# Kernel tuning notes

Hardware: AMD Instinct MI355X
Metric: run time of the kernel (lower is better)

Reference implementation:

```python
import jax, jax.numpy as jnp
import numpy as np

B = 16        # graphs per batch
N0 = 4096     # nodes per graph (equal-size graphs -> static TopK shapes)
DEG = 8       # avg degree
E = B * N0 * DEG
CW = 64
OUT = 256


def _seg_sum(vals, idx, n):
    return jax.ops.segment_sum(vals, idx, num_segments=n)


def _sage(x, src, dst, valid, wl, bl, wr, n):
    # PyG SAGEConv: lin_l(mean_{j->i} x_j) + lin_r(x_i); lin_r has no bias
    vf = valid.astype(x.dtype)
    msg = x[src] * vf[:, None]                     # [E, d]
    s = _seg_sum(msg, dst, n)
    cnt = _seg_sum(vf, dst, n)
    mean = s / jnp.maximum(cnt, 1.0)[:, None]
    return mean @ wl.T + bl + x @ wr.T


def _gcn(x, src, dst, valid, w, b, n):
    # PyG GCNConv: add self-loops, symmetric normalization
    h = x @ w.T
    vf = valid.astype(x.dtype)
    deg = 1.0 + _seg_sum(vf, dst, n)               # includes self-loop
    inv_sqrt = jax.lax.rsqrt(deg)
    norm = inv_sqrt[src] * inv_sqrt[dst] * vf      # [E]
    agg = _seg_sum(h[src] * norm[:, None], dst, n) + h * (1.0 / deg)[:, None]
    return agg + b


def _topk_pool(x, src, dst, valid, w, n_per_graph):
    # PyG TopKPooling: score = x@w/||w||, keep top ceil(ratio*n) per graph,
    # x' = x[perm] * tanh(score[perm]); reindex edges, drop edges with removed endpoints.
    k = (n_per_graph + 1) // 2
    score = (x @ w) / jnp.linalg.norm(w)
    vals, idx = jax.lax.top_k(score.reshape(B, n_per_graph), k)   # [B,k]
    offs = (jnp.arange(B, dtype=jnp.int32) * n_per_graph)[:, None]
    perm = (idx.astype(jnp.int32) + offs).reshape(-1)             # [B*k] global ids
    x_new = x[perm] * jnp.tanh(vals.reshape(-1))[:, None]
    new_idx = jnp.full((B * n_per_graph,), -1, dtype=jnp.int32).at[perm].set(
        jnp.arange(B * k, dtype=jnp.int32))
    s2, d2 = new_idx[src], new_idx[dst]
    valid2 = valid & (s2 >= 0) & (d2 >= 0)
    s2 = jnp.where(valid2, s2, 0)
    d2 = jnp.where(valid2, d2, 0)
    return x_new, s2, d2, valid2, k


def _readout(x, k):
    xg = x.reshape(B, k, -1)
    return jnp.concatenate([xg.max(axis=1), xg.mean(axis=1)], axis=1)  # [B, 2d]


def _forward(x, edge_src, edge_dst, w1_l, b1, w1_r, w2_l, b2, w2_r, w3_l, b3, w3_r,
             w4, b4, w5, b5, w6, b6, p1, p2, p3, p4, p5, p6,
             lw1, lb1, lw2, lb2, lw3, lb3):
    src, dst = edge_src, edge_dst
    valid = jnp.ones((E,), dtype=bool)
    n = N0
    sage_ps = [(w1_l, b1, w1_r), (w2_l, b2, w2_r), (w3_l, b3, w3_r)]
    gcn_ps = [(w4, b4), (w5, b5), (w6, b6)]
    pools = [p1, p2, p3, p4, p5, p6]
    h = x
    z = None
    for i in range(6):
        if i < 3:
            wl, bl, wr = sage_ps[i]
            h = jax.nn.relu(_sage(h, src, dst, valid, wl, bl, wr, B * n))
        else:
            w, b = gcn_ps[i - 3]
            h = jax.nn.relu(_gcn(h, src, dst, valid, w, b, B * n))
        h, src, dst, valid, n = _topk_pool(h, src, dst, valid, pools[i], n)
        r = _readout(h, n)
        z = r if z is None else z + r
    z = jax.nn.relu(z @ lw1.T + lb1)
    z = jax.nn.relu(z @ lw2.T + lb2)
    z = z @ lw3.T + lb3
    return jax.nn.softmax(z, axis=1)


def setup_inputs() -> dict:
    key = jax.random.key(0)
    ks = jax.random.split(key, 40)

    def nrm(k, shape, s=0.1):
        return jax.random.normal(k, shape, dtype=jnp.float32) * s

    # per-graph random edges (both endpoints inside the same graph block)
    epg = N0 * DEG
    src_l = jax.random.randint(ks[0], (B, epg), 0, N0, dtype=jnp.int32)
    dst_l = jax.random.randint(ks[1], (B, epg), 0, N0, dtype=jnp.int32)
    offs = (jnp.arange(B, dtype=jnp.int32) * N0)[:, None]
    inp = {
        'x': jax.random.normal(ks[2], (B * N0, 2), dtype=jnp.float32),
        'edge_src': (src_l + offs).reshape(-1),
        'edge_dst': (dst_l + offs).reshape(-1),
        'w1_l': nrm(ks[3], (CW, 2)), 'b1': nrm(ks[4], (CW,)), 'w1_r': nrm(ks[5], (CW, 2)),
        'w2_l': nrm(ks[6], (CW, CW)), 'b2': nrm(ks[7], (CW,)), 'w2_r': nrm(ks[8], (CW, CW)),
        'w3_l': nrm(ks[9], (CW, CW)), 'b3': nrm(ks[10], (CW,)), 'w3_r': nrm(ks[11], (CW, CW)),
        'w4': nrm(ks[12], (CW, CW)), 'b4': jnp.zeros((CW,), jnp.float32),
        'w5': nrm(ks[13], (CW, CW)), 'b5': jnp.zeros((CW,), jnp.float32),
        'w6': nrm(ks[14], (CW, CW)), 'b6': jnp.zeros((CW,), jnp.float32),
        'p1': nrm(ks[15], (CW,)), 'p2': nrm(ks[16], (CW,)), 'p3': nrm(ks[17], (CW,)),
        'p4': nrm(ks[18], (CW,)), 'p5': nrm(ks[19], (CW,)), 'p6': nrm(ks[20], (CW,)),
        'lw1': nrm(ks[21], (128, 2 * CW)), 'lb1': nrm(ks[22], (128,)),
        'lw2': nrm(ks[23], (64, 128)), 'lb2': nrm(ks[24], (64,)),
        'lw3': nrm(ks[25], (OUT, 64)), 'lb3': nrm(ks[26], (OUT,)),
    }
    return inp


def reference(x, edge_src, edge_dst, w1_l, b1, w1_r, w2_l, b2, w2_r, w3_l, b3, w3_r,
              w4, b4, w5, b5, w6, b6, p1, p2, p3, p4, p5, p6,
              lw1, lb1, lw2, lb2, lw3, lb3):
    return _forward(x, edge_src, edge_dst, w1_l, b1, w1_r, w2_l, b2, w2_r,
                    w3_l, b3, w3_r, w4, b4, w5, b5, w6, b6,
                    p1, p2, p3, p4, p5, p6, lw1, lb1, lw2, lb2, lw3, lb3)
```

## Files before the change

kernel.cpp:

```cpp
#include <hip/hip_runtime.h>
#include <math.h>

#define NB 16
#define N0 4096
#define NE 524288
#define CAPE 1280


static __global__ void k_count(const int* __restrict__ dst, int* __restrict__ cnt) {
  int e = blockIdx.x * 256 + threadIdx.x;
  if (e >= NE) return;
  atomicAdd(&cnt[dst[e]], 1);
}

static __global__ void k_fill0(const int* __restrict__ src, const int* __restrict__ dst,
                               int* __restrict__ cursor, int* __restrict__ list) {
  int e = blockIdx.x * 256 + threadIdx.x;
  if (e >= NE) return;
  int d = dst[e];
  int slot = atomicAdd(&cursor[d], 1);
  list[slot] = src[e];
}


static __global__ void k_scan1(const int* __restrict__ in, int* __restrict__ out,
                               int* __restrict__ bsum, int n) {
  __shared__ int ts[256];
  int base = blockIdx.x * 1024 + threadIdx.x * 4;
  int a0 = (base + 0 < n) ? in[base + 0] : 0;
  int a1 = (base + 1 < n) ? in[base + 1] : 0;
  int a2 = (base + 2 < n) ? in[base + 2] : 0;
  int a3 = (base + 3 < n) ? in[base + 3] : 0;
  int s = a0 + a1 + a2 + a3;
  ts[threadIdx.x] = s;
  __syncthreads();
  for (int off = 1; off < 256; off <<= 1) {
    int v = (threadIdx.x >= off) ? ts[threadIdx.x - off] : 0;
    __syncthreads();
    ts[threadIdx.x] += v;
    __syncthreads();
  }
  int excl = ts[threadIdx.x] - s;
  if (base + 0 < n) out[base + 0] = excl;
  excl += a0;
  if (base + 1 < n) out[base + 1] = excl;
  excl += a1;
  if (base + 2 < n) out[base + 2] = excl;
  excl += a2;
  if (base + 3 < n) out[base + 3] = excl;
  if (threadIdx.x == 255) bsum[blockIdx.x] = ts[255];
}

static __global__ void k_scan2(int* __restrict__ bsum, int nb) {
  __shared__ int t[64];
  int i = threadIdx.x;
  int v = (i < nb) ? bsum[i] : 0;
  t[i] = v;
  __syncthreads();
  for (int off = 1; off < 64; off <<= 1) {
    int u = (i >= off) ? t[i - off] : 0;
    __syncthreads();
    t[i] += u;
    __syncthreads();
  }
  if (i < nb) bsum[i] = t[i] - v;
}

static __global__ void k_scan3(int* __restrict__ out, int* __restrict__ out2,
                               const int* __restrict__ bsum, int n) {
  int i = blockIdx.x * 256 + threadIdx.x;
  if (i < n) {
    int v = out[i] + bsum[i >> 10];
    out[i] = v;
    if (out2) out2[i] = v;
  }
}


static __global__ void k_newcount(const int* __restrict__ perm, const int* __restrict__ offs,
                                  const int* __restrict__ cnt, const int* __restrict__ list,
                                  const int* __restrict__ newidx, int* __restrict__ ncnt,
                                  int newn) {
  int nn = blockIdx.x * 256 + threadIdx.x;
  if (nn >= newn) return;
  int old = perm[nn];
  int st = offs[old], c = cnt[old];
  int cc = 0;
  for (int j = 0; j < c; ++j) cc += (newidx[list[st + j]] >= 0);
  ncnt[nn] = cc;
}

static __global__ void k_newfill(const int* __restrict__ perm, const int* __restrict__ offs,
                                 const int* __restrict__ cnt, const int* __restrict__ list,
                                 const int* __restrict__ newidx, const int* __restrict__ noffs,
                                 int* __restrict__ nlist, int newn) {
  int nn = blockIdx.x * 256 + threadIdx.x;
  if (nn >= newn) return;
  int old = perm[nn];
  int st = offs[old], c = cnt[old];
  int pos = noffs[nn];
  for (int j = 0; j < c; ++j) {
    int s2 = newidx[list[st + j]];
    if (s2 >= 0) nlist[pos++] = s2;
  }
}


static __global__ void k_pnorm(const float* __restrict__ p0, const float* __restrict__ p1,
                               const float* __restrict__ p2, const float* __restrict__ p3,
                               const float* __restrict__ p4, const float* __restrict__ p5,
                               float* __restrict__ pnbuf) {
  const float* pp = p0;
  switch (blockIdx.x) {
    case 1: pp = p1; break;
    case 2: pp = p2; break;
    case 3: pp = p3; break;
    case 4: pp = p4; break;
    case 5: pp = p5; break;
    default: break;
  }
  double v = (double)pp[threadIdx.x];
  v *= v;
#pragma unroll
  for (int off = 1; off < 64; off <<= 1) v += __shfl_xor(v, off);
  if (threadIdx.x == 0) pnbuf[blockIdx.x] = (float)(1.0 / sqrt(v));
}


static __global__ void k_wprep(const float* __restrict__ w0, const float* __restrict__ w1,
                               const float* __restrict__ w2, const float* __restrict__ w3,
                               const float* __restrict__ w4, const float* __restrict__ w5,
                               const float* __restrict__ w6, float* __restrict__ wp) {
  const float* src = w0;
  switch (blockIdx.x) {
    case 1: src = w1; break;
    case 2: src = w2; break;
    case 3: src = w3; break;
    case 4: src = w4; break;
    case 5: src = w5; break;
    case 6: src = w6; break;
    default: break;
  }
  float* dst = wp + (size_t)blockIdx.x * 4096;
  const float4* w4p = (const float4*)src;
  for (int i4 = threadIdx.x; i4 < 1024; i4 += 256) {
    int o = i4 >> 4, db = (i4 & 15) << 2;
    float4 W = w4p[i4];
    float Wv[4] = {W.x, W.y, W.z, W.w};
    int og = o >> 2, o3 = o & 3;
#pragma unroll
    for (int j = 0; j < 4; ++j) {
      int d = db + j;
      dst[(d << 6) + (((og ^ (d & 15)) << 2) | o3)] = Wv[j];
    }
  }
}


static __global__ void k_sage_gather2(const float* __restrict__ x, const int* __restrict__ offs,
                                      const int* __restrict__ cnt, const int* __restrict__ list,
                                      float* __restrict__ mean, int ntot) {
  int v = blockIdx.x * 256 + threadIdx.x;
  if (v >= ntot) return;
  int st = offs[v], c = cnt[v];
  float s0 = 0.f, s1 = 0.f;
  for (int j = 0; j < c; ++j) {
    int s = list[st + j];
    s0 += x[s * 2 + 0];
    s1 += x[s * 2 + 1];
  }
  float inv = 1.0f / fmaxf((float)c, 1.0f);
  mean[v * 2 + 0] = s0 * inv;
  mean[v * 2 + 1] = s1 * inv;
}

static __global__ void k_sage0(const float* __restrict__ x, const float* __restrict__ mean,
                               const float* __restrict__ wl, const float* __restrict__ blv,
                               const float* __restrict__ wr, const float* __restrict__ pvec,
                               const float* __restrict__ pnbuf, float* __restrict__ h,
                               float* __restrict__ score, int ntot) {
  __shared__ float wlT[2][65], wrT[2][65];
  if (threadIdx.x < 128) {
    int o = threadIdx.x >> 1, d = threadIdx.x & 1;
    wlT[d][o] = wl[o * 2 + d];
    wrT[d][o] = wr[o * 2 + d];
  }
  __syncthreads();
  int o = threadIdx.x & 63, vl = threadIdx.x >> 6;
  int base = blockIdx.x * 16 + vl * 4;
  float pn = pnbuf[0];
  float psl = pvec[o];
#pragma unroll
  for (int r = 0; r < 4; ++r) {
    int v = base + r;
    if (v >= ntot) break;
    float acc = blv[o] + mean[v * 2 + 0] * wlT[0][o] + mean[v * 2 + 1] * wlT[1][o] +
                x[v * 2 + 0] * wrT[0][o] + x[v * 2 + 1] * wrT[1][o];
    float hval = fmaxf(acc, 0.0f);
    h[(size_t)v * 64 + o] = hval;
    double sc = (double)hval * (double)psl;
#pragma unroll
    for (int off = 1; off < 64; off <<= 1) sc += __shfl_xor(sc, off);
    if (o == 0) score[v] = (float)sc * pn;
  }
}

static __global__ __launch_bounds__(256) void k_sage_mm(
    const float* __restrict__ x, const int* __restrict__ offs, const int* __restrict__ cnt,
    const int* __restrict__ list, const float* __restrict__ wlT, const float* __restrict__ blv,
    const float* __restrict__ wrT, const float* __restrict__ pvec,
    const float* __restrict__ pnbuf, int pidx, float* __restrict__ h,
    float* __restrict__ score) {
  __shared__ float smem[8192];
  __shared__ float psh[64], bsh[64];
  __shared__ int lds_list[CAPE];
  float* xT = smem;
  float* mT = smem + 4096;
  int t = threadIdx.x;
  size_t nb = (size_t)((blockIdx.x & 7) * (gridDim.x >> 3) + (blockIdx.x >> 3));

  if (t < 64) {
    psh[t] = pvec[t];
    bsh[t] = blv[t];
  }
  const float4* x4 = (const float4*)(x + nb * 4096);
  for (int i = t; i < 1024; i += 256) {
    int node = i >> 4, db = (i & 15) << 2;
    float4 a = x4[i];
    float av[4] = {a.x, a.y, a.z, a.w};
    int ng = node >> 2, n0 = node & 3;
#pragma unroll
    for (int j = 0; j < 4; ++j) {
      int d = db + j;
      xT[(d << 6) + (((ng ^ (d & 15)) << 2) | n0)] = av[j];
    }
  }
  int gv0 = (int)nb * 64;
  int st0 = offs[gv0];
  int nedge = offs[gv0 + 63] + cnt[gv0 + 63] - st0;
  int ncap = (nedge < CAPE) ? nedge : CAPE;
  for (int e = t; e < ncap; e += 256) lds_list[e] = list[st0 + e];
  __syncthreads();

  {
    int lane = t & 63, w = t >> 6;
    int stq[16], cq[16];
    float accq[16];
    int cmax = 0;
#pragma unroll
    for (int q = 0; q < 16; ++q) {
      int gv = gv0 + w * 16 + q;
      stq[q] = offs[gv] - st0;
      cq[q] = cnt[gv];
      accq[q] = 0.f;
      cmax = max(cmax, cq[q]);
    }
    int ncl = (nedge > 0) ? (nedge - 1) : 0;
    for (int j = 0; j < cmax; ++j) {
#pragma unroll
      for (int q = 0; q < 16; ++q) {
        bool act = j < cq[q];
        int idx = stq[q] + (act ? j : 0);
        idx = (idx < ncl) ? idx : ncl;
        int sn = (idx < ncap) ? lds_list[idx] : list[st0 + idx];
        float xv = x[(size_t)(sn & 32767) * 64 + lane];
        accq[q] = act ? (accq[q] + xv) : accq[q];
      }
    }
#pragma unroll
    for (int q = 0; q < 16; ++q) {
      int node = w * 16 + q;
      float mval = accq[q] * (1.0f / fmaxf((float)cq[q], 1.0f));
      int col = (((node >> 2) ^ (lane & 15)) << 2) | (node & 3);
      mT[(lane << 6) + col] = mval;
    }
  }
  __syncthreads();

  int tx = t & 15, ty = t >> 4;
  float acc[4][4] = {};
#pragma unroll 4
  for (int k = 0; k < 64; ++k) {
    int s = k & 15;
    int ca = (tx ^ s) << 2, cb = (ty ^ s) << 2;
    const float4 a = *(const float4*)&xT[(k << 6) + ca];
    const float4 m = *(const float4*)&mT[(k << 6) + ca];
    const float4 L = *(const float4*)&wlT[(k << 6) + cb];
    const float4 R = *(const float4*)&wrT[(k << 6) + cb];
    float A[4] = {a.x, a.y, a.z, a.w}, M[4] = {m.x, m.y, m.z, m.w};
    float Lv[4] = {L.x, L.y, L.z, L.w}, Rv[4] = {R.x, R.y, R.z, R.w};
#pragma unroll
    for (int r = 0; r < 4; ++r)
#pragma unroll
      for (int c = 0; c < 4; ++c) acc[r][c] += M[r] * Lv[c] + A[r] * Rv[c];
  }

  float pn = pnbuf[pidx];
  float hv[4][4];
  double sp[4];
#pragma unroll
  for (int r = 0; r < 4; ++r) {
    sp[r] = 0.0;
#pragma unroll
    for (int c = 0; c < 4; ++c) {
      float v = fmaxf(acc[r][c] + bsh[(ty << 2) + c], 0.0f);
      hv[r][c] = v;
      sp[r] += (double)v * (double)psh[(ty << 2) + c];
    }
  }
  __syncthreads();
  float* hT = smem;
  double* sred = (double*)(smem + 4608);
#pragma unroll
  for (int r = 0; r < 4; ++r) {
    int node = (tx << 2) + r;
    int nk = node & 15;
#pragma unroll
    for (int c = 0; c < 4; ++c) hT[node * 68 + (((ty ^ nk) << 2) | c)] = hv[r][c];
    sred[(ty << 6) + node] = sp[r];
  }
  __syncthreads();
  float4* h4 = (float4*)(h + nb * 4096);
  for (int i = t; i < 1024; i += 256) {
    int node = i >> 4, q = i & 15;
    h4[i] = *(const float4*)&hT[node * 68 + ((q ^ (node & 15)) << 2)];
  }
  if (t < 64) {
    double ssum = 0.0;
    for (int g = 0; g < 16; ++g) ssum += sred[(g << 6) + t];
    score[nb * 64 + t] = (float)ssum * pn;
  }
}


static __global__ __launch_bounds__(256) void k_gcn_mm(const float* __restrict__ x,
                                                       const float* __restrict__ wT,
                                                       float* __restrict__ h1) {
  __shared__ float smem[4608];
  float* xT = smem;
  int t = threadIdx.x;
  size_t nb = blockIdx.x;
  const float4* x4 = (const float4*)(x + nb * 4096);
  for (int i = t; i < 1024; i += 256) {
    int node = i >> 4, db = (i & 15) << 2;
    float4 a = x4[i];
    float av[4] = {a.x, a.y, a.z, a.w};
    int ng = node >> 2, n0 = node & 3;
#pragma unroll
    for (int j = 0; j < 4; ++j) {
      int d = db + j;
      xT[(d << 6) + (((ng ^ (d & 15)) << 2) | n0)] = av[j];
    }
  }
  __syncthreads();
  int tx = t & 15, ty = t >> 4;
  float acc[4][4] = {};
#pragma unroll 4
  for (int k = 0; k < 64; ++k) {
    int s = k & 15;
    const float4 a = *(const float4*)&xT[(k << 6) + ((tx ^ s) << 2)];
    const float4 W = *(const float4*)&wT[(k << 6) + ((ty ^ s) << 2)];
    float A[4] = {a.x, a.y, a.z, a.w}, Wv[4] = {W.x, W.y, W.z, W.w};
#pragma unroll
    for (int r = 0; r < 4; ++r)
#pragma unroll
      for (int c = 0; c < 4; ++c) acc[r][c] += A[r] * Wv[c];
  }
  __syncthreads();
  float* hT = smem;
#pragma unroll
  for (int r = 0; r < 4; ++r) {
    int node = (tx << 2) + r;
    int nk = node & 15;
#pragma unroll
    for (int c = 0; c < 4; ++c) hT[node * 68 + (((ty ^ nk) << 2) | c)] = acc[r][c];
  }
  __syncthreads();
  float4* h4 = (float4*)(h1 + nb * 4096);
  for (int i = t; i < 1024; i += 256) {
    int node = i >> 4, q = i & 15;
    h4[i] = *(const float4*)&hT[node * 68 + ((q ^ (node & 15)) << 2)];
  }
}

static __global__ void k_gcn_gather(const float* __restrict__ h1, const int* __restrict__ offs,
                                    const int* __restrict__ cnt, const int* __restrict__ list,
                                    const float* __restrict__ b, const float* __restrict__ pvec,
                                    const float* __restrict__ pnbuf, int pidx,
                                    float* __restrict__ h, float* __restrict__ score, int ntot) {
  int lane = threadIdx.x & 63, vl = threadIdx.x >> 6;
  int v = blockIdx.x * 4 + vl;
  if (v >= ntot) return;
  int st = offs[v], c = cnt[v];
  float degv = 1.0f + (float)c;
  float ivd = 1.0f / sqrtf(degv);
  float acc = 0.f;
  for (int j = 0; j < c; ++j) {
    int s = list[st + j];
    float nrm = (1.0f / sqrtf(1.0f + (float)cnt[s])) * ivd;
    acc += h1[(size_t)s * 64 + lane] * nrm;
  }
  float outv = fmaxf(acc + h1[(size_t)v * 64 + lane] * (1.0f / degv) + b[lane], 0.0f);
  h[(size_t)v * 64 + lane] = outv;
  double sc = (double)outv * (double)pvec[lane];
#pragma unroll
  for (int off = 1; off < 64; off <<= 1) sc += __shfl_xor(sc, off);
  if (lane == 0) score[v] = (float)sc * pnbuf[pidx];
}


static __global__ void k_chunksort(const float* __restrict__ score,
                                   unsigned long long* __restrict__ runs, int n_per, int k,
                                   int* __restrict__ newidx, int* __restrict__ perm, int single) {
  extern __shared__ unsigned long long sk[];
  int CH = blockDim.x;
  int g0 = blockIdx.x * CH;
  int b = g0 / n_per;
  int i = threadIdx.x;
  int gi = g0 + i;
  int li = gi - b * n_per;
  unsigned u = __float_as_uint(score[gi]);
  unsigned s = (u & 0x80000000u) ? u : ~(u | 0x80000000u);
  sk[i] = ((unsigned long long)s << 32) | (unsigned)li;
  __syncthreads();
  for (int ksz = 2; ksz <= CH; ksz <<= 1) {
    for (int j = ksz >> 1; j > 0; j >>= 1) {
      int ixj = i ^ j;
      if (ixj > i) {
        unsigned long long a = sk[i], c = sk[ixj];
        bool up = ((i & ksz) == 0);
        if ((a > c) == up) {
          sk[i] = c;
          sk[ixj] = a;
        }
      }
      __syncthreads();
    }
  }
  if (!single) {
    runs[gi] = sk[i];
  } else {
    int r = i;
    int idx = (int)(sk[r] & 0xFFFFFFFFu);
    int gidx = b * n_per + idx;
    if (r < k) {
      perm[b * k + r] = gidx;
      newidx[gidx] = b * k + r;
    } else {
      newidx[gidx] = -1;
    }
  }
}

static __global__ void k_merge(const unsigned long long* __restrict__ in,
                               unsigned long long* __restrict__ out, int L, int ntot, int n_per,
                               int k, int* __restrict__ newidx, int* __restrict__ perm,
                               int final) {
  int g = blockIdx.x * 256 + threadIdx.x;
  if (g >= ntot) return;
  unsigned long long key = in[g];
  int pair = g / (2 * L);
  int base = pair * 2 * L;
  int t = g - base;
  const unsigned long long* sib;
  int p;
  if (t < L) {
    sib = in + base + L;
    p = t;
  } else {
    sib = in + base;
    p = t - L;
  }
  int lo = 0, hi = L;
  while (lo < hi) {
    int mid = (lo + hi) >> 1;
    lo = (sib[mid] < key) ? mid + 1 : lo;
    hi = (sib[mid] < key) ? hi : mid;
  }
  int pos = p + lo;
  if (!final) {
    out[base + pos] = key;
  } else {
    int b = base / n_per;
    int idx = (int)(key & 0xFFFFFFFFu);
    int gidx = b * n_per + idx;
    if (pos < k) {
      perm[b * k + pos] = gidx;
      newidx[gidx] = b * k + pos;
    } else {
      newidx[gidx] = -1;
    }
  }
}


static __global__ __launch_bounds__(1024) void k_gather_ro(
    const float* __restrict__ h, const float* __restrict__ score, const int* __restrict__ perm,
    float* __restrict__ xnew, float* __restrict__ pmax, float* __restrict__ psum) {
  __shared__ float tile[64 * 68];
  __shared__ float pm[16][65], ps[16][65];
  int t = threadIdx.x;
  int node = t >> 4, q = t & 15;
  int nn = blockIdx.x * 64 + node;
  int old = perm[nn];
  float tm = tanhf(score[old]);
  float4 v = *(const float4*)&h[(size_t)old * 64 + q * 4];
  v.x *= tm;
  v.y *= tm;
  v.z *= tm;
  v.w *= tm;
  *(float4*)&xnew[(size_t)nn * 64 + q * 4] = v;
  *(float4*)&tile[node * 68 + ((q ^ (node & 15)) << 2)] = v;
  __syncthreads();
  int slot = t >> 6, d = t & 63;
  int q2 = d >> 2, i3 = d & 3;
  float m = -INFINITY, s = 0.f;
#pragma unroll
  for (int r = 0; r < 4; ++r) {
    int nd = slot * 4 + r;
    float val = tile[nd * 68 + (((q2 ^ (nd & 15)) << 2) | i3)];
    m = fmaxf(m, val);
    s += val;
  }
  pm[slot][d] = m;
  ps[slot][d] = s;
  __syncthreads();
  if (t < 64) {
    float mm = -INFINITY, ss = 0.f;
#pragma unroll
    for (int sl = 0; sl < 16; ++sl) {
      mm = fmaxf(mm, pm[sl][t]);
      ss += ps[sl][t];
    }
    pmax[(size_t)blockIdx.x * 64 + t] = mm;
    psum[(size_t)blockIdx.x * 64 + t] = ss;
  }
}

static __global__ void k_readout_comb(const float* __restrict__ pmax,
                                      const float* __restrict__ psum, float* __restrict__ z,
                                      int k, int nch) {
  int b = blockIdx.x, d = threadIdx.x;
  float m = -INFINITY, s = 0.0f;
  for (int c = 0; c < nch; ++c) {
    m = fmaxf(m, pmax[((size_t)b * nch + c) * 64 + d]);
    s += psum[((size_t)b * nch + c) * 64 + d];
  }
  z[b * 128 + d] += m;
  z[b * 128 + 64 + d] += s / (float)k;
}


static __global__ void k_mlp(const float* __restrict__ z, const float* __restrict__ lw1,
                             const float* __restrict__ lb1, const float* __restrict__ lw2,
                             const float* __restrict__ lb2, const float* __restrict__ lw3,
                             const float* __restrict__ lb3, float* __restrict__ out) {
  __shared__ float zs[128], t1[128], t2[64], t3[256], red[256];
  int b = blockIdx.x, tid = threadIdx.x;
  if (tid < 128) zs[tid] = z[b * 128 + tid];
  __syncthreads();
  if (tid < 128) {
    double a = 0.0;
    for (int d = 0; d < 128; ++d) a += (double)lw1[tid * 128 + d] * (double)zs[d];
    t1[tid] = fmaxf((float)a + lb1[tid], 0.0f);
  }
  __syncthreads();
  if (tid < 64) {
    double a = 0.0;
    for (int d = 0; d < 128; ++d) a += (double)lw2[tid * 128 + d] * (double)t1[d];
    t2[tid] = fmaxf((float)a + lb2[tid], 0.0f);
  }
  __syncthreads();
  {
    double a = 0.0;
    for (int d = 0; d < 64; ++d) a += (double)lw3[tid * 64 + d] * (double)t2[d];
    t3[tid] = (float)a + lb3[tid];
  }
  __syncthreads();
  red[tid] = t3[tid];
  __syncthreads();
  for (int s = 128; s > 0; s >>= 1) {
    if (tid < s) red[tid] = fmaxf(red[tid], red[tid + s]);
    __syncthreads();
  }
  float mx = red[0];
  __syncthreads();
  float e = expf(t3[tid] - mx);
  red[tid] = e;
  __syncthreads();
  for (int s = 128; s > 0; s >>= 1) {
    if (tid < s) red[tid] += red[tid + s];
    __syncthreads();
  }
  out[b * 256 + tid] = e / red[0];
}


extern "C" void kernel_launch(void* const* d_in, const int* in_sizes, int n_in,
                              void* d_out, int out_size, void* d_ws, size_t ws_size,
                              hipStream_t stream) {
  const float* x0 = (const float*)d_in[0];
  const int* esrc0 = (const int*)d_in[1];
  const int* edst0 = (const int*)d_in[2];
  const float* WL[3] = {(const float*)d_in[3], (const float*)d_in[6], (const float*)d_in[9]};
  const float* BL[3] = {(const float*)d_in[4], (const float*)d_in[7], (const float*)d_in[10]};
  const float* WR[3] = {(const float*)d_in[5], (const float*)d_in[8], (const float*)d_in[11]};
  const float* WG[3] = {(const float*)d_in[12], (const float*)d_in[14], (const float*)d_in[16]};
  const float* BG[3] = {(const float*)d_in[13], (const float*)d_in[15], (const float*)d_in[17]};
  const float* P[6] = {(const float*)d_in[18], (const float*)d_in[19], (const float*)d_in[20],
                       (const float*)d_in[21], (const float*)d_in[22], (const float*)d_in[23]};
  const float* lw1 = (const float*)d_in[24];
  const float* lb1 = (const float*)d_in[25];
  const float* lw2 = (const float*)d_in[26];
  const float* lb2 = (const float*)d_in[27];
  const float* lw3 = (const float*)d_in[28];
  const float* lb3 = (const float*)d_in[29];

  char* ws = (char*)d_ws;
  size_t off = 0;
  auto alloc = [&](size_t bytes) -> void* {
    void* p = ws + off;
    off += (bytes + 255) & ~(size_t)255;
    return p;
  };
  float* hA = (float*)alloc((size_t)65536 * 64 * 4);
  float* hB = (float*)alloc((size_t)32768 * 64 * 4);
  float* mean = (float*)alloc((size_t)65536 * 2 * 4);
  float* tmp = (float*)alloc((size_t)8192 * 64 * 4);
  float* score = (float*)alloc((size_t)65536 * 4);
  int* newidx = (int*)alloc((size_t)65536 * 4);
  int* perm = (int*)alloc((size_t)32768 * 4);
  int* cntA = (int*)alloc((size_t)65536 * 4);
  int* cntB = (int*)alloc((size_t)65536 * 4);
  int* offsA = (int*)alloc((size_t)65536 * 4);
  int* offsB = (int*)alloc((size_t)65536 * 4);
  int* cursor = (int*)alloc((size_t)65536 * 4);
  int* bsum = (int*)alloc((size_t)64 * 4);
  int* listA = (int*)alloc((size_t)NE * 4);
  int* listB = (int*)alloc((size_t)NE * 4);
  float* z = (float*)alloc((size_t)16 * 128 * 4);
  float* pmax = (float*)alloc((size_t)NB * 32 * 64 * 4);
  float* psum = (float*)alloc((size_t)NB * 32 * 64 * 4);
  unsigned long long* keyA = (unsigned long long*)alloc((size_t)65536 * 8);
  unsigned long long* keyB = (unsigned long long*)alloc((size_t)65536 * 8);
  float* pnbuf = (float*)alloc((size_t)64 * 4);
  float* wp = (float*)alloc((size_t)7 * 4096 * 4);
  if (off > ws_size) return;

  auto scan = [&](int* cntp, int* offsp, int* curp, int n) {
    int nblk = (n + 1023) / 1024;
    k_scan1<<<nblk, 256, 0, stream>>>(cntp, offsp, bsum, n);
    k_scan2<<<1, 64, 0, stream>>>(bsum, nblk);
    k_scan3<<<(n + 255) / 256, 256, 0, stream>>>(offsp, curp, bsum, n);
  };

  hipMemsetAsync(z, 0, 16 * 128 * 4, stream);
  k_pnorm<<<6, 64, 0, stream>>>(P[0], P[1], P[2], P[3], P[4], P[5], pnbuf);
  k_wprep<<<7, 256, 0, stream>>>(WL[1], WR[1], WL[2], WR[2], WG[0], WG[1], WG[2], wp);

  hipMemsetAsync(cntA, 0, (size_t)65536 * 4, stream);
  k_count<<<NE / 256, 256, 0, stream>>>(edst0, cntA);
  scan(cntA, offsA, cursor, 65536);
  k_fill0<<<NE / 256, 256, 0, stream>>>(esrc0, edst0, cursor, listA);

  const float* xcur = x0;
  int* ccnt = cntA;
  int* coffs = offsA;
  int* clist = listA;

  for (int i = 0; i < 6; ++i) {
    int n_per = N0 >> i;
    int ntot = NB * n_per;
    int k = n_per >> 1;

    if (i == 0) {
      k_sage_gather2<<<(ntot + 255) / 256, 256, 0, stream>>>(xcur, coffs, ccnt, clist, mean, ntot);
      k_sage0<<<(ntot + 15) / 16, 256, 0, stream>>>(xcur, mean, WL[0], BL[0], WR[0], P[0], pnbuf,
                                                    hA, score, ntot);
    } else if (i < 3) {
      const float* wlp = wp + (size_t)((i - 1) * 2 + 0) * 4096;
      const float* wrp = wp + (size_t)((i - 1) * 2 + 1) * 4096;
      k_sage_mm<<<ntot / 64, 256, 0, stream>>>(xcur, coffs, ccnt, clist, wlp, BL[i], wrp, P[i],
                                               pnbuf, i, hA, score);
    } else {
      int g = i - 3;
      k_gcn_mm<<<ntot / 64, 256, 0, stream>>>(xcur, wp + (size_t)(4 + g) * 4096, tmp);
      k_gcn_gather<<<(ntot + 3) / 4, 256, 0, stream>>>(tmp, coffs, ccnt, clist, BG[g], P[i],
                                                       pnbuf, i, hA, score, ntot);
    }

    int CH = (n_per < 1024) ? n_per : 1024;
    int single = (CH == n_per) ? 1 : 0;
    k_chunksort<<<ntot / CH, CH, (size_t)CH * 8, stream>>>(score, keyA, n_per, k, newidx, perm,
                                                           single);
    if (!single) {
      unsigned long long* cur = keyA;
      unsigned long long* nxt = keyB;
      for (int L = CH; L * 2 <= n_per; L <<= 1) {
        int fin = (L * 2 == n_per) ? 1 : 0;
        k_merge<<<(ntot + 255) / 256, 256, 0, stream>>>(cur, nxt, L, ntot, n_per, k, newidx, perm,
                                                        fin);
        unsigned long long* t2 = cur;
        cur = nxt;
        nxt = t2;
      }
    }

    int nch = k / 64;
    k_gather_ro<<<NB * nch, 1024, 0, stream>>>(hA, score, perm, hB, pmax, psum);

    if (i < 5) {
      int newn = NB * k;
      int* ncnt = (i & 1) ? cntA : cntB;
      int* noffs = (i & 1) ? offsA : offsB;
      int* nlist = (i & 1) ? listA : listB;
      k_newcount<<<(newn + 255) / 256, 256, 0, stream>>>(perm, coffs, ccnt, clist, newidx, ncnt,
                                                         newn);
      scan(ncnt, noffs, nullptr, newn);
      k_newfill<<<(newn + 255) / 256, 256, 0, stream>>>(perm, coffs, ccnt, clist, newidx, noffs,
                                                        nlist, newn);
      ccnt = ncnt;
      coffs = noffs;
      clist = nlist;
    }

    k_readout_comb<<<NB, 64, 0, stream>>>(pmax, psum, z, k, nch);
    xcur = hB;
  }

  k_mlp<<<NB, 256, 0, stream>>>(z, lw1, lb1, lw2, lb2, lw3, lb3, (float*)d_out);
}
```

Before: 401.4 us.

## Merge small kernels to cut launches and widen sage_mm blocks to 512 threads

Folds scan2 into scan3 using a wavefront shuffle scan, merges pnorm and wprep into one launch, and merges the newcount work into the pooling gather kernel as extra blocks. Per-level readout combining moves into the final MLP kernel, which also removes the z memset. k_sage_mm now runs 512 threads per block, each thread covering a 2x4 output tile and 8 nodes' gathers instead of 4x4 and 16. The goal is fewer kernel launches and more parallelism in the sage layers, at the cost of some redundant block-sum scans and lower per-thread reuse.

```diff
diff --git a/kernel.cpp b/kernel.cpp
--- a/kernel.cpp
+++ b/kernel.cpp
@@ -51,44 +51,28 @@
   if (threadIdx.x == 255) bsum[blockIdx.x] = ts[255];
 }
 
-static __global__ void k_scan2(int* __restrict__ bsum, int nb) {
-  __shared__ int t[64];
-  int i = threadIdx.x;
-  int v = (i < nb) ? bsum[i] : 0;
-  t[i] = v;
-  __syncthreads();
-  for (int off = 1; off < 64; off <<= 1) {
-    int u = (i >= off) ? t[i - off] : 0;
-    __syncthreads();
-    t[i] += u;
-    __syncthreads();
-  }
-  if (i < nb) bsum[i] = t[i] - v;
-}
-
 static __global__ void k_scan3(int* __restrict__ out, int* __restrict__ out2,
-                               const int* __restrict__ bsum, int n) {
-  int i = blockIdx.x * 256 + threadIdx.x;
+                               const int* __restrict__ bsum, int n, int nblk) {
+  __shared__ int sb[64];
+  int t = threadIdx.x;
+  if (t < 64) {
+    int v = (t < nblk) ? bsum[t] : 0;
+    int p = v;
+    for (int off = 1; off < 64; off <<= 1) {
+      int u = __shfl_up(p, off);
+      if (t >= off) p += u;
+    }
+    sb[t] = p - v;
+  }
+  __syncthreads();
+  int i = blockIdx.x * 256 + t;
   if (i < n) {
-    int v = out[i] + bsum[i >> 10];
+    int v = out[i] + sb[i >> 10];
     out[i] = v;
     if (out2) out2[i] = v;
   }
 }
 
-
-static __global__ void k_newcount(const int* __restrict__ perm, const int* __restrict__ offs,
-                                  const int* __restrict__ cnt, const int* __restrict__ list,
-                                  const int* __restrict__ newidx, int* __restrict__ ncnt,
-                                  int newn) {
-  int nn = blockIdx.x * 256 + threadIdx.x;
-  if (nn >= newn) return;
-  int old = perm[nn];
-  int st = offs[old], c = cnt[old];
-  int cc = 0;
-  for (int j = 0; j < c; ++j) cc += (newidx[list[st + j]] >= 0);
-  ncnt[nn] = cc;
-}
 
 static __global__ void k_newfill(const int* __restrict__ perm, const int* __restrict__ offs,
                                  const int* __restrict__ cnt, const int* __restrict__ list,
@@ -106,52 +90,54 @@
 }
 
 
-static __global__ void k_pnorm(const float* __restrict__ p0, const float* __restrict__ p1,
-                               const float* __restrict__ p2, const float* __restrict__ p3,
-                               const float* __restrict__ p4, const float* __restrict__ p5,
-                               float* __restrict__ pnbuf) {
-  const float* pp = p0;
-  switch (blockIdx.x) {
-    case 1: pp = p1; break;
-    case 2: pp = p2; break;
-    case 3: pp = p3; break;
-    case 4: pp = p4; break;
-    case 5: pp = p5; break;
-    default: break;
-  }
-  double v = (double)pp[threadIdx.x];
-  v *= v;
-#pragma unroll
-  for (int off = 1; off < 64; off <<= 1) v += __shfl_xor(v, off);
-  if (threadIdx.x == 0) pnbuf[blockIdx.x] = (float)(1.0 / sqrt(v));
-}
-
-
-static __global__ void k_wprep(const float* __restrict__ w0, const float* __restrict__ w1,
-                               const float* __restrict__ w2, const float* __restrict__ w3,
-                               const float* __restrict__ w4, const float* __restrict__ w5,
-                               const float* __restrict__ w6, float* __restrict__ wp) {
-  const float* src = w0;
-  switch (blockIdx.x) {
-    case 1: src = w1; break;
-    case 2: src = w2; break;
-    case 3: src = w3; break;
-    case 4: src = w4; break;
-    case 5: src = w5; break;
-    case 6: src = w6; break;
-    default: break;
-  }
-  float* dst = wp + (size_t)blockIdx.x * 4096;
-  const float4* w4p = (const float4*)src;
-  for (int i4 = threadIdx.x; i4 < 1024; i4 += 256) {
-    int o = i4 >> 4, db = (i4 & 15) << 2;
-    float4 W = w4p[i4];
-    float Wv[4] = {W.x, W.y, W.z, W.w};
-    int og = o >> 2, o3 = o & 3;
-#pragma unroll
-    for (int j = 0; j < 4; ++j) {
-      int d = db + j;
-      dst[(d << 6) + (((og ^ (d & 15)) << 2) | o3)] = Wv[j];
+static __global__ void k_pw(const float* __restrict__ p0, const float* __restrict__ p1,
+                            const float* __restrict__ p2, const float* __restrict__ p3,
+                            const float* __restrict__ p4, const float* __restrict__ p5,
+                            const float* __restrict__ w0, const float* __restrict__ w1,
+                            const float* __restrict__ w2, const float* __restrict__ w3,
+                            const float* __restrict__ w4, const float* __restrict__ w5,
+                            const float* __restrict__ w6, float* __restrict__ pnbuf,
+                            float* __restrict__ wp) {
+  if (blockIdx.x < 6) {
+    if (threadIdx.x >= 64) return;
+    const float* pp = p0;
+    switch (blockIdx.x) {
+      case 1: pp = p1; break;
+      case 2: pp = p2; break;
+      case 3: pp = p3; break;
+      case 4: pp = p4; break;
+      case 5: pp = p5; break;
+      default: break;
+    }
+    double v = (double)pp[threadIdx.x];
+    v *= v;
+#pragma unroll
+    for (int off = 1; off < 64; off <<= 1) v += __shfl_xor(v, off);
+    if (threadIdx.x == 0) pnbuf[blockIdx.x] = (float)(1.0 / sqrt(v));
+  } else {
+    int wi = blockIdx.x - 6;
+    const float* src = w0;
+    switch (wi) {
+      case 1: src = w1; break;
+      case 2: src = w2; break;
+      case 3: src = w3; break;
+      case 4: src = w4; break;
+      case 5: src = w5; break;
+      case 6: src = w6; break;
+      default: break;
+    }
+    float* dst = wp + (size_t)wi * 4096;
+    const float4* w4p = (const float4*)src;
+    for (int i4 = threadIdx.x; i4 < 1024; i4 += 256) {
+      int o = i4 >> 4, db = (i4 & 15) << 2;
+      float4 W = w4p[i4];
+      float Wv[4] = {W.x, W.y, W.z, W.w};
+      int og = o >> 2, o3 = o & 3;
+#pragma unroll
+      for (int j = 0; j < 4; ++j) {
+        int d = db + j;
+        dst[(d << 6) + (((og ^ (d & 15)) << 2) | o3)] = Wv[j];
+      }
     }
   }
 }
@@ -205,7 +191,7 @@
   }
 }
 
-static __global__ __launch_bounds__(256) void k_sage_mm(
+static __global__ __launch_bounds__(512) void k_sage_mm(
     const float* __restrict__ x, const int* __restrict__ offs, const int* __restrict__ cnt,
     const int* __restrict__ list, const float* __restrict__ wlT, const float* __restrict__ blv,
     const float* __restrict__ wrT, const float* __restrict__ pvec,
@@ -224,7 +210,7 @@
     bsh[t] = blv[t];
   }
   const float4* x4 = (const float4*)(x + nb * 4096);
-  for (int i = t; i < 1024; i += 256) {
+  for (int i = t; i < 1024; i += 512) {
     int node = i >> 4, db = (i & 15) << 2;
     float4 a = x4[i];
     float av[4] = {a.x, a.y, a.z, a.w};
@@ -239,17 +225,17 @@
   int st0 = offs[gv0];
   int nedge = offs[gv0 + 63] + cnt[gv0 + 63] - st0;
   int ncap = (nedge < CAPE) ? nedge : CAPE;
-  for (int e = t; e < ncap; e += 256) lds_list[e] = list[st0 + e];
+  for (int e = t; e < ncap; e += 512) lds_list[e] = list[st0 + e];
   __syncthreads();
 
   {
     int lane = t & 63, w = t >> 6;
-    int stq[16], cq[16];
-    float accq[16];
+    int stq[8], cq[8];
+    float accq[8];
     int cmax = 0;
 #pragma unroll
-    for (int q = 0; q < 16; ++q) {
-      int gv = gv0 + w * 16 + q;
+    for (int q = 0; q < 8; ++q) {
+      int gv = gv0 + w * 8 + q;
       stq[q] = offs[gv] - st0;
       cq[q] = cnt[gv];
       accq[q] = 0.f;
@@ -258,7 +244,7 @@
     int ncl = (nedge > 0) ? (nedge - 1) : 0;
     for (int j = 0; j < cmax; ++j) {
 #pragma unroll
-      for (int q = 0; q < 16; ++q) {
+      for (int q = 0; q < 8; ++q) {
         bool act = j < cq[q];
         int idx = stq[q] + (act ? j : 0);
         idx = (idx < ncl) ? idx : ncl;
@@ -268,8 +254,8 @@
       }
     }
 #pragma unroll
-    for (int q = 0; q < 16; ++q) {
-      int node = w * 16 + q;
+    for (int q = 0; q < 8; ++q) {
+      int node = w * 8 + q;
       float mval = accq[q] * (1.0f / fmaxf((float)cq[q], 1.0f));
       int col = (((node >> 2) ^ (lane & 15)) << 2) | (node & 3);
       mT[(lane << 6) + col] = mval;
@@ -278,50 +264,51 @@
   __syncthreads();
 
   int tx = t & 15, ty = t >> 4;
-  float acc[4][4] = {};
+  int ng = ty >> 1, n0 = (ty & 1) << 1;
+  float acc[2][4] = {};
 #pragma unroll 4
   for (int k = 0; k < 64; ++k) {
     int s = k & 15;
-    int ca = (tx ^ s) << 2, cb = (ty ^ s) << 2;
-    const float4 a = *(const float4*)&xT[(k << 6) + ca];
-    const float4 m = *(const float4*)&mT[(k << 6) + ca];
-    const float4 L = *(const float4*)&wlT[(k << 6) + cb];
-    const float4 R = *(const float4*)&wrT[(k << 6) + cb];
-    float A[4] = {a.x, a.y, a.z, a.w}, M[4] = {m.x, m.y, m.z, m.w};
+    int ca = (((ng ^ s) << 2) | n0);
+    const float2 a2 = *(const float2*)&xT[(k << 6) + ca];
+    const float2 m2 = *(const float2*)&mT[(k << 6) + ca];
+    const float4 L = *(const float4*)&wlT[(k << 6) + ((tx ^ s) << 2)];
+    const float4 R = *(const float4*)&wrT[(k << 6) + ((tx ^ s) << 2)];
+    float A[2] = {a2.x, a2.y}, M[2] = {m2.x, m2.y};
     float Lv[4] = {L.x, L.y, L.z, L.w}, Rv[4] = {R.x, R.y, R.z, R.w};
 #pragma unroll
-    for (int r = 0; r < 4; ++r)
+    for (int r = 0; r < 2; ++r)
 #pragma unroll
       for (int c = 0; c < 4; ++c) acc[r][c] += M[r] * Lv[c] + A[r] * Rv[c];
   }
 
   float pn = pnbuf[pidx];
-  float hv[4][4];
-  double sp[4];
-#pragma unroll
-  for (int r = 0; r < 4; ++r) {
+  float hv[2][4];
+  double sp[2];
+#pragma unroll
+  for (int r = 0; r < 2; ++r) {
     sp[r] = 0.0;
 #pragma unroll
     for (int c = 0; c < 4; ++c) {
-      float v = fmaxf(acc[r][c] + bsh[(ty << 2) + c], 0.0f);
+      float v = fmaxf(acc[r][c] + bsh[(tx << 2) + c], 0.0f);
       hv[r][c] = v;
-      sp[r] += (double)v * (double)psh[(ty << 2) + c];
+      sp[r] += (double)v * (double)psh[(tx << 2) + c];
     }
   }
   __syncthreads();
   float* hT = smem;
   double* sred = (double*)(smem + 4608);
 #pragma unroll
-  for (int r = 0; r < 4; ++r) {
-    int node = (tx << 2) + r;
+  for (int r = 0; r < 2; ++r) {
+    int node = (ty << 1) + r;
     int nk = node & 15;
 #pragma unroll
-    for (int c = 0; c < 4; ++c) hT[node * 68 + (((ty ^ nk) << 2) | c)] = hv[r][c];
-    sred[(ty << 6) + node] = sp[r];
+    for (int c = 0; c < 4; ++c) hT[node * 68 + (((tx ^ nk) << 2) | c)] = hv[r][c];
+    sred[(tx << 6) + node] = sp[r];
   }
   __syncthreads();
   float4* h4 = (float4*)(h + nb * 4096);
-  for (int i = t; i < 1024; i += 256) {
+  for (int i = t; i < 1024; i += 512) {
     int node = i >> 4, q = i & 15;
     h4[i] = *(const float4*)&hT[node * 68 + ((q ^ (node & 15)) << 2)];
   }
@@ -494,12 +481,24 @@
 }
 
 
-static __global__ __launch_bounds__(1024) void k_gather_ro(
+static __global__ __launch_bounds__(1024) void k_pool_post(
     const float* __restrict__ h, const float* __restrict__ score, const int* __restrict__ perm,
-    float* __restrict__ xnew, float* __restrict__ pmax, float* __restrict__ psum) {
+    float* __restrict__ xnew, float* __restrict__ pmax, float* __restrict__ psum, int base,
+    const int* __restrict__ offs, const int* __restrict__ cnt, const int* __restrict__ list,
+    const int* __restrict__ newidx, int* __restrict__ ncnt, int newn, int G1) {
   __shared__ float tile[64 * 68];
   __shared__ float pm[16][65], ps[16][65];
   int t = threadIdx.x;
+  if ((int)blockIdx.x >= G1) {
+    int nn = ((int)blockIdx.x - G1) * 1024 + t;
+    if (nn >= newn) return;
+    int old = perm[nn];
+    int st = offs[old], c = cnt[old];
+    int cc = 0;
+    for (int j = 0; j < c; ++j) cc += (newidx[list[st + j]] >= 0);
+    ncnt[nn] = cc;
+    return;
+  }
   int node = t >> 4, q = t & 15;
   int nn = blockIdx.x * 64 + node;
   int old = perm[nn];
@@ -532,32 +531,42 @@
       mm = fmaxf(mm, pm[sl][t]);
       ss += ps[sl][t];
     }
-    pmax[(size_t)blockIdx.x * 64 + t] = mm;
-    psum[(size_t)blockIdx.x * 64 + t] = ss;
-  }
-}
-
-static __global__ void k_readout_comb(const float* __restrict__ pmax,
-                                      const float* __restrict__ psum, float* __restrict__ z,
-                                      int k, int nch) {
-  int b = blockIdx.x, d = threadIdx.x;
-  float m = -INFINITY, s = 0.0f;
-  for (int c = 0; c < nch; ++c) {
-    m = fmaxf(m, pmax[((size_t)b * nch + c) * 64 + d]);
-    s += psum[((size_t)b * nch + c) * 64 + d];
-  }
-  z[b * 128 + d] += m;
-  z[b * 128 + 64 + d] += s / (float)k;
-}
-
-
-static __global__ void k_mlp(const float* __restrict__ z, const float* __restrict__ lw1,
-                             const float* __restrict__ lb1, const float* __restrict__ lw2,
-                             const float* __restrict__ lb2, const float* __restrict__ lw3,
-                             const float* __restrict__ lb3, float* __restrict__ out) {
+    pmax[(size_t)(base + blockIdx.x) * 64 + t] = mm;
+    psum[(size_t)(base + blockIdx.x) * 64 + t] = ss;
+  }
+}
+
+
+static __global__ void k_mlp(const float* __restrict__ pmax, const float* __restrict__ psum,
+                             const float* __restrict__ lw1, const float* __restrict__ lb1,
+                             const float* __restrict__ lw2, const float* __restrict__ lb2,
+                             const float* __restrict__ lw3, const float* __restrict__ lb3,
+                             float* __restrict__ out) {
   __shared__ float zs[128], t1[128], t2[64], t3[256], red[256];
   int b = blockIdx.x, tid = threadIdx.x;
-  if (tid < 128) zs[tid] = z[b * 128 + tid];
+  const int baseL[6] = {0, 512, 768, 896, 960, 992};
+  const int nchL[6] = {32, 16, 8, 4, 2, 1};
+  const int kkL[6] = {2048, 1024, 512, 256, 128, 64};
+  if (tid < 64) {
+    float zm = 0.f;
+    for (int i = 0; i < 6; ++i) {
+      float m = -INFINITY;
+      for (int c = 0; c < nchL[i]; ++c)
+        m = fmaxf(m, pmax[(size_t)(baseL[i] + b * nchL[i] + c) * 64 + tid]);
+      zm += m;
+    }
+    zs[tid] = zm;
+  } else if (tid < 128) {
+    int d = tid - 64;
+    float zsum = 0.f;
+    for (int i = 0; i < 6; ++i) {
+      float s = 0.f;
+      for (int c = 0; c < nchL[i]; ++c)
+        s += psum[(size_t)(baseL[i] + b * nchL[i] + c) * 64 + d];
+      zsum += s / (float)kkL[i];
+    }
+    zs[tid] = zsum;
+  }
   __syncthreads();
   if (tid < 128) {
     double a = 0.0;
@@ -638,9 +647,8 @@
   int* bsum = (int*)alloc((size_t)64 * 4);
   int* listA = (int*)alloc((size_t)NE * 4);
   int* listB = (int*)alloc((size_t)NE * 4);
-  float* z = (float*)alloc((size_t)16 * 128 * 4);
-  float* pmax = (float*)alloc((size_t)NB * 32 * 64 * 4);
-  float* psum = (float*)alloc((size_t)NB * 32 * 64 * 4);
+  float* pmax = (float*)alloc((size_t)1024 * 64 * 4);
+  float* psum = (float*)alloc((size_t)1024 * 64 * 4);
   unsigned long long* keyA = (unsigned long long*)alloc((size_t)65536 * 8);
   unsigned long long* keyB = (unsigned long long*)alloc((size_t)65536 * 8);
   float* pnbuf = (float*)alloc((size_t)64 * 4);
@@ -650,13 +658,11 @@
   auto scan = [&](int* cntp, int* offsp, int* curp, int n) {
     int nblk = (n + 1023) / 1024;
     k_scan1<<<nblk, 256, 0, stream>>>(cntp, offsp, bsum, n);
-    k_scan2<<<1, 64, 0, stream>>>(bsum, nblk);
-    k_scan3<<<(n + 255) / 256, 256, 0, stream>>>(offsp, curp, bsum, n);
+    k_scan3<<<(n + 255) / 256, 256, 0, stream>>>(offsp, curp, bsum, n, nblk);
   };
 
-  hipMemsetAsync(z, 0, 16 * 128 * 4, stream);
-  k_pnorm<<<6, 64, 0, stream>>>(P[0], P[1], P[2], P[3], P[4], P[5], pnbuf);
-  k_wprep<<<7, 256, 0, stream>>>(WL[1], WR[1], WL[2], WR[2], WG[0], WG[1], WG[2], wp);
+  k_pw<<<13, 256, 0, stream>>>(P[0], P[1], P[2], P[3], P[4], P[5], WL[1], WR[1], WL[2], WR[2],
+                               WG[0], WG[1], WG[2], pnbuf, wp);
 
   hipMemsetAsync(cntA, 0, (size_t)65536 * 4, stream);
   k_count<<<NE / 256, 256, 0, stream>>>(edst0, cntA);
@@ -667,6 +673,7 @@
   int* ccnt = cntA;
   int* coffs = offsA;
   int* clist = listA;
+  const int baseL[6] = {0, 512, 768, 896, 960, 992};
 
   for (int i = 0; i < 6; ++i) {
     int n_per = N0 >> i;
@@ -680,7 +687,7 @@
     } else if (i < 3) {
       const float* wlp = wp + (size_t)((i - 1) * 2 + 0) * 4096;
       const float* wrp = wp + (size_t)((i - 1) * 2 + 1) * 4096;
-      k_sage_mm<<<ntot / 64, 256, 0, stream>>>(xcur, coffs, ccnt, clist, wlp, BL[i], wrp, P[i],
+      k_sage_mm<<<ntot / 64, 512, 0, stream>>>(xcur, coffs, ccnt, clist, wlp, BL[i], wrp, P[i],
                                                pnbuf, i, hA, score);
     } else {
       int g = i - 3;
@@ -707,15 +714,16 @@
     }
 
     int nch = k / 64;
-    k_gather_ro<<<NB * nch, 1024, 0, stream>>>(hA, score, perm, hB, pmax, psum);
+    int G1 = NB * nch;
+    int newn = (i < 5) ? NB * k : 0;
+    int* ncnt = (i & 1) ? cntA : cntB;
+    int G2 = (newn > 0) ? (newn + 1023) / 1024 : 0;
+    k_pool_post<<<G1 + G2, 1024, 0, stream>>>(hA, score, perm, hB, pmax, psum, baseL[i], coffs,
+                                              ccnt, clist, newidx, ncnt, newn, G1);
 
     if (i < 5) {
-      int newn = NB * k;
-      int* ncnt = (i & 1) ? cntA : cntB;
       int* noffs = (i & 1) ? offsA : offsB;
       int* nlist = (i & 1) ? listA : listB;
-      k_newcount<<<(newn + 255) / 256, 256, 0, stream>>>(perm, coffs, ccnt, clist, newidx, ncnt,
-                                                         newn);
       scan(ncnt, noffs, nullptr, newn);
       k_newfill<<<(newn + 255) / 256, 256, 0, stream>>>(perm, coffs, ccnt, clist, newidx, noffs,
                                                         nlist, newn);
@@ -724,9 +732,8 @@
       clist = nlist;
     }
 
-    k_readout_comb<<<NB, 64, 0, stream>>>(pmax, psum, z, k, nch);
     xcur = hB;
   }
 
-  k_mlp<<<NB, 256, 0, stream>>>(z, lw1, lb1, lw2, lb2, lw3, lb3, (float*)d_out);
-}
+  k_mlp<<<NB, 256, 0, stream>>>(pmax, psum, lw1, lb1, lw2, lb2, lw3, lb3, (float*)d_out);
+}
```

Measured after the change: 351.6 us. -12.4%, faster.
